# Kernel tuning notes

Hardware: AMD Instinct MI355X
Metric: run time of the kernel (lower is better)

## Reference

```python
import jax, jax.numpy as jnp
import numpy as np

DN = ('NCHW', 'OIHW', 'NCHW')
LN_EPS = 1e-5
L2_EPS = 1e-12


def dwconv(x, w, pad):
    # depthwise conv: x [b,c,h,w], w [c,1,kh,kw]
    return jax.lax.conv_general_dilated(
        x, w, (1, 1), [(pad, pad), (pad, pad)],
        dimension_numbers=DN, feature_group_count=x.shape[1])


def l2norm(x):
    n = jnp.sqrt(jnp.sum(x * x, axis=-1, keepdims=True))
    return x / jnp.maximum(n, L2_EPS)


def setup_inputs() -> dict:
    key = jax.random.key(0)
    L, c, heads, mult = 2, 512, 8, 4
    cm = c * mult
    ks = jax.random.split(key, 18)
    rn = lambda k, s, sc=0.02: jax.random.normal(k, s, jnp.float32) * sc
    return {
        'x': jax.random.normal(ks[0], (2, c, 128, 128), jnp.float32),
        'Wq': rn(ks[1], (L, c, c)),
        'Wk': rn(ks[2], (L, c, c)),
        'Wv': rn(ks[3], (L, c, c)),
        'rescale': jnp.ones((L, heads, 1, 1), jnp.float32),
        'proj_W': rn(ks[4], (L, c, c)),
        'proj_b': jnp.zeros((L, c), jnp.float32),
        'pos_w1': rn(ks[5], (L, c, 1, 3, 3)),
        'pos_w2': rn(ks[6], (L, c, 1, 3, 3)),
        'ln_g': jnp.ones((L, c), jnp.float32),
        'ln_b': jnp.zeros((L, c), jnp.float32),
        'w1': rn(ks[7], (L, cm, c)),
        'dw1': rn(ks[8], (L, cm // 4, 1, 1, 1), 0.1),
        'dw3': rn(ks[9], (L, cm // 4, 1, 3, 3), 0.1),
        'dw5': rn(ks[10], (L, cm // 4, 1, 5, 5), 0.1),
        'dw7': rn(ks[11], (L, cm // 4, 1, 7, 7), 0.1),
        'w2': rn(ks[12], (L, c, cm)),
    }


def reference(x, Wq, Wk, Wv, rescale, proj_W, proj_b, pos_w1, pos_w2,
              ln_g, ln_b, w1, dw1, dw3, dw5, dw7, w2):
    b, c, H, W = x.shape
    heads = rescale.shape[1]
    d = c // heads
    n = H * W
    x = x.transpose(0, 2, 3, 1)  # [b,H,W,c]
    for l in range(Wq.shape[0]):
        # ---- S_MSA (channel-wise transposed attention) ----
        xf = x.reshape(b, n, c)
        q_inp = xf @ Wq[l]
        k_inp = xf @ Wk[l]
        v_inp = xf @ Wv[l]
        # [b,n,heads,d] -> [b,heads,d,n]
        to_hd = lambda t: t.reshape(b, n, heads, d).transpose(0, 2, 3, 1)
        q, k, v = to_hd(q_inp), to_hd(k_inp), to_hd(v_inp)
        q = l2norm(q)
        k = l2norm(k)
        attn = jnp.einsum('bhdn,bhen->bhde', k, q) * rescale[l]  # [b,h,d,d]
        attn = jax.nn.softmax(attn, axis=-1)
        o = jnp.einsum('bhde,bhen->bhdn', attn, v)
        o = o.transpose(0, 3, 1, 2).reshape(b, n, c)  # [b,n,heads*d]
        out_c = (o @ proj_W[l] + proj_b[l]).reshape(b, H, W, c)
        # positional branch on v_inp
        vimg = v_inp.reshape(b, H, W, c).transpose(0, 3, 1, 2)
        p = dwconv(vimg, pos_w1[l], 1)
        p = jax.nn.gelu(p, approximate=False)
        p = dwconv(p, pos_w2[l], 1)
        x = x + out_c + p.transpose(0, 2, 3, 1)
        # ---- PreNorm + MS_FFN ----
        mu = x.mean(-1, keepdims=True)
        var = jnp.mean((x - mu) ** 2, axis=-1, keepdims=True)
        xn = (x - mu) / jnp.sqrt(var + LN_EPS) * ln_g[l] + ln_b[l]
        y = xn.transpose(0, 3, 1, 2)  # [b,c,H,W]
        y = jnp.einsum('oc,bchw->bohw', w1[l], y)  # [b,4c,H,W]
        y1, y2, y3, y4 = jnp.split(y, 4, axis=1)
        o1 = dwconv(y1, dw1[l], 0)
        o2 = dwconv(y2, dw3[l], 1)
        o3 = dwconv(y3, dw5[l], 2)
        o4 = dwconv(y4, dw7[l], 3)
        o = jnp.concatenate([o1, o2, o3, o4], axis=1) + y
        o = jnp.einsum('oc,bchw->bohw', w2[l], o)  # [b,c,H,W]
        x = x + o.transpose(0, 2, 3, 1)
    return x.transpose(0, 3, 1, 2)
```

## Files before the change

### kernel.cpp

```cpp
#include <hip/hip_runtime.h>
#include <math.h>

typedef unsigned short u16;
typedef short bf16x8 __attribute__((ext_vector_type(8)));
typedef float f32x4 __attribute__((ext_vector_type(4)));
typedef float f32x2 __attribute__((ext_vector_type(2)));

__device__ __forceinline__ float bf2f(u16 h) {
    union { unsigned u; float f; } v; v.u = ((unsigned)h) << 16; return v.f;
}
__device__ __forceinline__ u16 f2bf(float f) {
    union { float f; unsigned u; } v; v.f = f;
    unsigned r = v.u + 0x7fffu + ((v.u >> 16) & 1u);
    return (u16)(r >> 16);
}
__device__ __forceinline__ f32x2 up2(unsigned u) {
    union { unsigned v; float f; } lo, hi;
    lo.v = u << 16; hi.v = u & 0xffff0000u;
    f32x2 r; r.x = lo.f; r.y = hi.f; return r;
}
__device__ __forceinline__ f32x2 unpk(unsigned u) { return up2(u); }
__device__ __forceinline__ f32x4 unpk(uint2 u) {
    f32x2 a = up2(u.x), b = up2(u.y);
    f32x4 r; r.x = a.x; r.y = a.y; r.z = b.x; r.w = b.y; return r;
}
__device__ __forceinline__ unsigned pkbf(f32x2 v) {
    return (unsigned)f2bf(v.x) | ((unsigned)f2bf(v.y) << 16);
}
__device__ __forceinline__ uint2 pkbf(f32x4 v) {
    uint2 r;
    r.x = (unsigned)f2bf(v.x) | ((unsigned)f2bf(v.y) << 16);
    r.y = (unsigned)f2bf(v.z) | ((unsigned)f2bf(v.w) << 16);
    return r;
}
__device__ __forceinline__ float gl(float v) {
    return 0.5f * v * (1.f + erff(v * 0.70710678118654752f));
}

__device__ __forceinline__ void gload_lds16(const u16* g, u16* l) {
    __builtin_amdgcn_global_load_lds(
        (const __attribute__((address_space(1))) void*)g,
        (__attribute__((address_space(3))) void*)l, 16, 0, 0);
}

template<int N> struct VecT;
template<> struct VecT<2> { typedef f32x2 T; typedef unsigned U; };
template<> struct VecT<4> { typedef f32x4 T; typedef uint2 U; };

#define CH    512
#define NPIX  16384
#define PTOT  32768
#define NHEAD 8

__global__ void transpose_k(const float* __restrict__ in, float* outF, u16* outB,
                            int R, int Cc, size_t ibs, size_t obs)
{
    __shared__ float tile[32][33];
    int z = blockIdx.z;
    const float* ip = in + (size_t)z * ibs;
    int c0 = blockIdx.x * 32, r0 = blockIdx.y * 32;
    int tx = threadIdx.x, ty = threadIdx.y;
#pragma unroll
    for (int j = 0; j < 4; j++)
        tile[ty + j * 8][tx] = ip[(size_t)(r0 + ty + j * 8) * Cc + c0 + tx];
    __syncthreads();
#pragma unroll
    for (int j = 0; j < 4; j++) {
        int orow = c0 + ty + j * 8, ocol = r0 + tx;
        float v = tile[tx][ty + j * 8];
        size_t o = (size_t)z * obs + (size_t)orow * R + ocol;
        if (outF) outF[o] = v;
        if (outB) outB[o] = f2bf(v);
    }
}

__global__ void transpose16_k(const u16* __restrict__ in, u16* __restrict__ out,
                              int R, int Cc, size_t ibs, size_t obs)
{
    __shared__ u16 tile[32][34];
    int z = blockIdx.z;
    const u16* ip = in + (size_t)z * ibs;
    int c0 = blockIdx.x * 32, r0 = blockIdx.y * 32;
    int tx = threadIdx.x, ty = threadIdx.y;
#pragma unroll
    for (int j = 0; j < 4; j++)
        tile[ty + j * 8][tx] = ip[(size_t)(r0 + ty + j * 8) * Cc + c0 + tx];
    __syncthreads();
#pragma unroll
    for (int j = 0; j < 4; j++)
        out[(size_t)z * obs + (size_t)(c0 + ty + j * 8) * R + r0 + tx] = tile[tx][ty + j * 8];
}

__global__ void cvt_bf16_k(const float* __restrict__ in, u16* __restrict__ out)
{
    size_t i = ((size_t)blockIdx.x * 256 + threadIdx.x) * 4;
    float4 v = *(const float4*)&in[i];
    uint2 st;
    st.x = (unsigned)f2bf(v.x) | ((unsigned)f2bf(v.y) << 16);
    st.y = (unsigned)f2bf(v.z) | ((unsigned)f2bf(v.w) << 16);
    *(uint2*)&out[i] = st;
}

__global__ void cvtw2_k(const float* __restrict__ in, const float* __restrict__ dw1,
                        u16* __restrict__ out)
{
    size_t i = ((size_t)blockIdx.x * 256 + threadIdx.x) * 4;
    int cp = (int)(i & 2047);
    int l = (int)(i >> 20);
    int src; bool ps = false;
    if (cp < 512)       src = 1024 + cp;
    else if (cp < 1024) src = 1536 + (cp - 512);
    else if (cp < 1536) { src = cp - 1024; ps = true; }
    else                src = 512 + (cp - 1536);
    float4 v = *(const float4*)&in[(i & ~(size_t)2047) + src];
    if (ps) {
        v.x *= 1.f + dw1[l * 512 + src];
        v.y *= 1.f + dw1[l * 512 + src + 1];
        v.z *= 1.f + dw1[l * 512 + src + 2];
        v.w *= 1.f + dw1[l * 512 + src + 3];
    }
    uint2 st;
    st.x = (unsigned)f2bf(v.x) | ((unsigned)f2bf(v.y) << 16);
    st.y = (unsigned)f2bf(v.z) | ((unsigned)f2bf(v.w) << 16);
    *(uint2*)&out[i] = st;
}

__global__ __launch_bounds__(512) void gemm5_k(
    const u16* __restrict__ A, const u16* __restrict__ Bw,
    int K, int ldb, int Nn, int rowsPerBatch, int bStride, int kChunk,
    const float* __restrict__ bias, const float* resid,
    float* outF, u16* outB, const u16* __restrict__ addB)
{
    __shared__ __attribute__((aligned(16))) u16 smem[6 * 4096];
    u16* Asb = smem;
    u16* Bsb = smem + 3 * 4096;
    int tid = threadIdx.x;

    int gx = gridDim.x;
    int nwg = gx * gridDim.y;
    int lin = blockIdx.y * gx + blockIdx.x;
    int swz = lin;
    if ((nwg & 7) == 0) swz = (lin & 7) * (nwg >> 3) + (lin >> 3);
    int bx = swz % gx, by = swz / gx;

    int rowBase = by * 128, colBase = bx * 128;
    const u16* Bp = Bw + (size_t)(rowBase / rowsPerBatch) * bStride;

    int kb = 0, ke = K;
    float* outFp = outF;
    if (kChunk) {
        kb = blockIdx.z * kChunk; ke = kb + kChunk;
        outFp = outF + (size_t)blockIdx.z * (size_t)gridDim.y * 128 * Nn;
    }

    f32x4 acc[4][2] = {};
    int lane = tid & 63, wave = tid >> 6;
    int wr = wave >> 2, wc = wave & 3;
    int lm = lane & 15, lk = lane >> 4;

    int row0 = tid >> 2;
    int kc   = ((tid ^ (tid >> 3)) & 3) * 8;
    int lb0  = (tid & ~63) * 8;

    const size_t aR0 = (size_t)(rowBase + row0) * K;
    const size_t bR0 = (size_t)(colBase + row0) * ldb;

    auto STAGE = [&](int bsel, int k0) {
        gload_lds16(&A [aR0 + k0 + kc], Asb + bsel * 4096 + lb0);
        gload_lds16(&Bp[bR0 + k0 + kc], Bsb + bsel * 4096 + lb0);
    };

    const int nsteps = (ke - kb) >> 5;
    STAGE(0, kb);
    STAGE(1, kb + 32);
    const int sl = (lk ^ ((lm >> 1) & 3)) * 8;

    for (int s = 0; s < nsteps; ++s) {
        asm volatile("s_waitcnt vmcnt(2)" ::: "memory");
        __builtin_amdgcn_s_barrier();
        __builtin_amdgcn_sched_barrier(0);
        int kpf = kb + ((s + 2 < nsteps) ? (s + 2) : (nsteps - 1)) * 32;
        STAGE((s + 2) % 3, kpf);

        const u16* Ab = Asb + (s % 3) * 4096;
        const u16* Bb = Bsb + (s % 3) * 4096;
        bf16x8 af[4], bfr[2];
#pragma unroll
        for (int mt = 0; mt < 4; mt++)
            af[mt] = *(const bf16x8*)&Ab[(wr * 64 + mt * 16 + lm) * 32 + sl];
#pragma unroll
        for (int nt = 0; nt < 2; nt++)
            bfr[nt] = *(const bf16x8*)&Bb[(wc * 32 + nt * 16 + lm) * 32 + sl];
        __builtin_amdgcn_s_setprio(1);
#pragma unroll
        for (int mt = 0; mt < 4; mt++)
#pragma unroll
            for (int nt = 0; nt < 2; nt++)
                acc[mt][nt] = __builtin_amdgcn_mfma_f32_16x16x32_bf16(
                    af[mt], bfr[nt], acc[mt][nt], 0, 0, 0);
        __builtin_amdgcn_s_setprio(0);
    }

    {
        float* smf = (float*)smem;
        constexpr int PADW = 132;
        const int erow = tid >> 5;
        const int ecol = (tid & 31) * 4;
        for (int hf = 0; hf < 4; ++hf) {
            __syncthreads();
            if (wr == (hf >> 1)) {
                int mtb = (hf & 1) * 2;
#pragma unroll
                for (int m2 = 0; m2 < 2; m2++) {
#pragma unroll
                    for (int nt = 0; nt < 2; nt++) {
                        int lr = m2 * 16 + lk * 4;
                        int lc = wc * 32 + nt * 16 + lm;
#pragma unroll
                        for (int r = 0; r < 4; r++)
                            smf[(lr + r) * PADW + lc] = acc[mtb + m2][nt][r];
                    }
                }
            }
            __syncthreads();
#pragma unroll
            for (int p = 0; p < 2; p++) {
                int lrow = erow + p * 16;
                int grow = rowBase + hf * 32 + lrow;
                int gcol = colBase + ecol;
                f32x4 v = *(f32x4*)&smf[lrow * PADW + ecol];
                if (bias) {
                    v.x += bias[gcol];     v.y += bias[gcol + 1];
                    v.z += bias[gcol + 2]; v.w += bias[gcol + 3];
                }
                size_t o = (size_t)grow * Nn + gcol;
                if (resid) { f32x4 rv = *(const f32x4*)&resid[o]; v += rv; }
                if (addB)  { f32x4 av = unpk(*(const uint2*)&addB[o]); v += av; }
                if (outFp) *(f32x4*)&outFp[o] = v;
                if (outB) { uint2 pk = pkbf(v); *(uint2*)&outB[o] = pk; }
            }
        }
    }
}

template<int TM, int TN>
__global__ __launch_bounds__(256) void gemm_nt_k(
    const u16* __restrict__ A, const u16* __restrict__ Bw,
    int K, int ldb, int Nn, int rowsPerBatch, int bStride, int kChunk,
    const float* __restrict__ bias, const float* resid,
    float* outF, u16* outB, const u16* __restrict__ addB)
{
    constexpr int MT = TM / 32;
    constexpr int NT = TN / 32;
    constexpr int ABUF = TM * 32;
    constexpr int BBUF = TN * 32;
    __shared__ __attribute__((aligned(16))) u16 smem[2 * ABUF + 2 * BBUF];
    u16* Asb = smem;
    u16* Bsb = smem + 2 * ABUF;
    int tid = threadIdx.x;

    int gx = gridDim.x;
    int nwg = gx * gridDim.y;
    int lin = blockIdx.y * gx + blockIdx.x;
    int swz = lin;
    if ((nwg & 7) == 0) swz = (lin & 7) * (nwg >> 3) + (lin >> 3);
    int bx = swz % gx, by = swz / gx;

    int rowBase = by * TM, colBase = bx * TN;
    const u16* Bp = Bw + (size_t)(rowBase / rowsPerBatch) * bStride;

    int kb = 0, ke = K;
    float* outFp = outF;
    if (kChunk) {
        kb = blockIdx.z * kChunk; ke = kb + kChunk;
        outFp = outF + (size_t)blockIdx.z * (size_t)gridDim.y * TM * Nn;
    }

    f32x4 acc[MT][NT] = {};
    int lane = tid & 63, wave = tid >> 6;
    int wr = wave >> 1, wc = wave & 1;
    int lm = lane & 15, lk = lane >> 4;

    int row0 = tid >> 2;
    int kc   = ((tid ^ (tid >> 3)) & 3) * 8;
    int lb0  = (tid & ~63) * 8;

    const size_t aR0 = (size_t)(rowBase + row0) * K;
    const size_t bR0 = (size_t)(colBase + row0) * ldb;
    const size_t aR1 = (size_t)(rowBase + 64 + row0) * K;
    const size_t bR1 = (size_t)(colBase + 64 + row0) * ldb;

    auto STAGE = [&](int bsel, int k0) {
        gload_lds16(&A [aR0 + k0 + kc], Asb + bsel * ABUF + lb0);
        gload_lds16(&Bp[bR0 + k0 + kc], Bsb + bsel * BBUF + lb0);
        if constexpr (TM == 128)
            gload_lds16(&A [aR1 + k0 + kc], Asb + bsel * ABUF + lb0 + 2048);
        if constexpr (TN == 128)
            gload_lds16(&Bp[bR1 + k0 + kc], Bsb + bsel * BBUF + lb0 + 2048);
    };

    STAGE(0, kb);
    __syncthreads();
    int buf = 0;
    const int sl = (lk ^ ((lm >> 1) & 3)) * 8;

    for (int k0 = kb; k0 < ke; k0 += 32) {
        if (k0 + 32 < ke) STAGE(buf ^ 1, k0 + 32);
        const u16* Ab = Asb + buf * ABUF;
        const u16* Bb = Bsb + buf * BBUF;
        bf16x8 af[MT], bfr[NT];
#pragma unroll
        for (int mt = 0; mt < MT; mt++)
            af[mt] = *(const bf16x8*)&Ab[(wr * (TM / 2) + mt * 16 + lm) * 32 + sl];
#pragma unroll
        for (int nt = 0; nt < NT; nt++)
            bfr[nt] = *(const bf16x8*)&Bb[(wc * (TN / 2) + nt * 16 + lm) * 32 + sl];
#pragma unroll
        for (int mt = 0; mt < MT; mt++)
#pragma unroll
            for (int nt = 0; nt < NT; nt++)
                acc[mt][nt] = __builtin_amdgcn_mfma_f32_16x16x32_bf16(
                    af[mt], bfr[nt], acc[mt][nt], 0, 0, 0);
        __syncthreads();
        buf ^= 1;
    }

    {
        float* smf = (float*)smem;
        constexpr int PADW = TN + 4;
        constexpr int HALVES = TM / 32;
        constexpr int HPW = (MT / 2 > 0) ? MT / 2 : 1;
        const int erow = tid >> 5;
        const int ecol = (tid & 31) * 4;
        for (int hf = 0; hf < HALVES; ++hf) {
            __syncthreads();
            if (wr == hf / HPW) {
                int mtb = (hf % HPW) * 2;
#pragma unroll
                for (int m2 = 0; m2 < 2; m2++) {
#pragma unroll
                    for (int nt = 0; nt < NT; nt++) {
                        int lr = m2 * 16 + lk * 4;
                        int lc = wc * (TN / 2) + nt * 16 + lm;
#pragma unroll
                        for (int r = 0; r < 4; r++)
                            smf[(lr + r) * PADW + lc] = acc[mtb + m2][nt][r];
                    }
                }
            }
            __syncthreads();
#pragma unroll
            for (int p = 0; p < 4; p++) {
                int lrow = erow + p * 8;
                int grow = rowBase + hf * 32 + lrow;
                int gcol = colBase + ecol;
                f32x4 v = *(f32x4*)&smf[lrow * PADW + ecol];
                if (bias) {
                    v.x += bias[gcol];     v.y += bias[gcol + 1];
                    v.z += bias[gcol + 2]; v.w += bias[gcol + 3];
                }
                size_t o = (size_t)grow * Nn + gcol;
                if (resid) { f32x4 rv = *(const f32x4*)&resid[o]; v += rv; }
                if (addB)  { f32x4 av = unpk(*(const uint2*)&addB[o]); v += av; }
                if (outFp) *(f32x4*)&outFp[o] = v;
                if (outB) { uint2 pk = pkbf(v); *(uint2*)&outB[o] = pk; }
            }
        }
    }
}

__global__ void sreduce_k(const float* __restrict__ Sp, u16* __restrict__ Sbf)
{
    int i = blockIdx.x * 256 + threadIdx.x;
    float s = 0.f;
#pragma unroll
    for (int z = 0; z < 8; z++) s += Sp[(size_t)z * 524288 + i];
    Sbf[i] = f2bf(s);
}

__global__ void nrm_k(const float* __restrict__ w, const float* __restrict__ Tf,
                      float* __restrict__ inv)
{
    int idx = blockIdx.x * 256 + threadIdx.x;
    int e = idx & 511, b = idx >> 9;
    float s = 0.f;
    for (int c = 0; c < 512; c++)
        s += w[c * 512 + e] * Tf[(size_t)(b * 512 + c) * 512 + e];
    s = fmaxf(s, 0.f);
    inv[b * 512 + e] = 1.f / fmaxf(sqrtf(s), 1e-12f);
}

__global__ __launch_bounds__(256) void gsmall_k(
    const float* __restrict__ T2f, const float* __restrict__ Wq,
    const float* __restrict__ qinv, const float* __restrict__ kinv,
    const float* __restrict__ resc, float* __restrict__ att)
{
    __shared__ float t2l[64][64], wql[64][64];
    int t = threadIdx.x, h = blockIdx.x, b = blockIdx.y;
    const int eg = (t & 15) * 4;
    const int dg = (t >> 4) * 4;
    f32x4 acc[4] = {};
    for (int c0 = 0; c0 < 512; c0 += 64) {
        __syncthreads();
        for (int i = t; i < 4096; i += 256) {
            int cc = i >> 6, j = i & 63;
            t2l[cc][j] = T2f[(size_t)(b * 512 + c0 + cc) * 512 + h * 64 + j];
            wql[cc][j] = Wq[(size_t)(c0 + cc) * 512 + h * 64 + j];
        }
        __syncthreads();
        for (int cc = 0; cc < 64; cc++) {
            f32x4 qv = *(f32x4*)&wql[cc][eg];
            f32x4 dv = *(f32x4*)&t2l[cc][dg];
            acc[0] += dv.x * qv;
            acc[1] += dv.y * qv;
            acc[2] += dv.z * qv;
            acc[3] += dv.w * qv;
        }
    }
    float rs = resc[h];
    f32x4 qn = *(const f32x4*)&qinv[b * 512 + h * 64 + eg];
    float* ap = att + (size_t)(b * 8 + h) * 4096;
#pragma unroll
    for (int dj = 0; dj < 4; dj++) {
        int d = dg + dj;
        float kn = kinv[b * 512 + h * 64 + d];
        f32x4 v = acc[dj] * kn;
        v = v * qn;
        v.x *= rs; v.y *= rs; v.z *= rs; v.w *= rs;
        float m = fmaxf(fmaxf(v.x, v.y), fmaxf(v.z, v.w));
        for (int off = 1; off <= 8; off <<= 1) m = fmaxf(m, __shfl_xor(m, off));
        f32x4 ev;
        ev.x = expf(v.x - m); ev.y = expf(v.y - m);
        ev.z = expf(v.z - m); ev.w = expf(v.w - m);
        float s = ev.x + ev.y + ev.z + ev.w;
        for (int off = 1; off <= 8; off <<= 1) s += __shfl_xor(s, off);
        f32x4 r;
        r.x = ev.x / s; r.y = ev.y / s; r.z = ev.z / s; r.w = ev.w / s;
        *(f32x4*)&ap[d * 64 + eg] = r;
    }
}

__global__ __launch_bounds__(256) void mbuild_k(const float* __restrict__ attn,
                                                const float* __restrict__ projW,
                                                u16* Mnt)
{
    __shared__ float at[64][64];
    __shared__ float pw[64][64];
    int t = threadIdx.x;
    int h = blockIdx.x, b = blockIdx.y, ot = blockIdx.z;
    const float* ap = attn + (size_t)(b * NHEAD + h) * 4096;
    for (int i = t; i < 4096; i += 256) {
        at[i >> 6][i & 63] = ap[i];
        pw[i >> 6][i & 63] = projW[(size_t)(h * 64 + (i >> 6)) * CH + ot * 64 + (i & 63)];
    }
    __syncthreads();
    const int eg = (t & 15) * 4;
    const int rg = (t >> 4) * 4;
    f32x4 acc[4] = {};
    for (int dd = 0; dd < 64; dd++) {
        f32x4 av = *(f32x4*)&at[dd][eg];
        f32x4 pv = *(f32x4*)&pw[dd][rg];
        acc[0] += pv.x * av;
        acc[1] += pv.y * av;
        acc[2] += pv.z * av;
        acc[3] += pv.w * av;
    }
#pragma unroll
    for (int j = 0; j < 4; j++) {
        uint2 pk = pkbf(acc[j]);
        *(uint2*)&Mnt[(size_t)b * (CH * CH)
                      + (size_t)(ot * 64 + rg + j) * CH + h * 64 + eg] = pk;
    }
}

template<int KS, int YS, int CPT, bool GELU_F, bool RESID, bool ACC, int SI, int SO>
__global__ __launch_bounds__(256, 1) void dwreg_k(
    const u16* __restrict__ in, const float* __restrict__ w,
    u16* __restrict__ outB, float* __restrict__ outAdd)
{
    constexpr int PAD = KS / 2;
    typedef typename VecT<CPT>::T fv;
    typedef typename VecT<CPT>::U uv;
    const int tid = threadIdx.x;
    const int cbase = (CPT == 4) ? ((tid & 127) * 4) : (tid * 2);
    const int x     = (CPT == 4) ? ((int)blockIdx.x * 2 + (tid >> 7)) : (int)blockIdx.x;
    const int y0 = blockIdx.y * YS;
    const int b  = blockIdx.z;
    const size_t bi = (size_t)b * NPIX * SI + cbase;
    const size_t bo = (size_t)b * NPIX * SO + cbase;

    fv wv[KS * KS];
#pragma unroll
    for (int t = 0; t < KS * KS; t++) {
        fv vv;
        vv.x = w[(cbase + 0) * KS * KS + t];
        vv.y = w[(cbase + 1) * KS * KS + t];
        if constexpr (CPT == 4) {
            vv.z = w[(cbase + 2) * KS * KS + t];
            vv.w = w[(cbase + 3) * KS * KS + t];
        }
        wv[t] = vv;
    }

    fv win[KS][KS];
    uv tmp[KS];

    auto rowload = [&](int t) {
        int yy = y0 - PAD + t;
        bool rv = ((unsigned)yy < 128u);
#pragma unroll
        for (int kx = 0; kx < KS; kx++) {
            int xx = x + kx - PAD;
            uv u = {};
            if (rv && ((unsigned)xx < 128u))
                u = *(const uv*)&in[bi + ((size_t)yy * 128 + xx) * SI];
            tmp[kx] = u;
        }
    };
    auto unpackrow = [&](int slot) {
#pragma unroll
        for (int kx = 0; kx < KS; kx++) win[slot][kx] = unpk(tmp[kx]);
    };

#pragma unroll
    for (int t = 0; t < KS - 1; t++) { rowload(t); unpackrow(t); }
    rowload(KS - 1);

    for (int i0 = 0; i0 < YS; i0 += KS) {
#pragma unroll
        for (int j = 0; j < KS; j++) {
            int i = i0 + j;
            if (i >= YS) break;
            unpackrow((j + KS - 1) % KS);
            if (i < YS - 1) rowload(i + KS);
            fv r = {};
#pragma unroll
            for (int ky = 0; ky < KS; ky++)
#pragma unroll
                for (int kx = 0; kx < KS; kx++)
                    r += win[(j + ky) % KS][kx] * wv[ky * KS + kx];
            if (GELU_F) {
                r.x = gl(r.x); r.y = gl(r.y);
                if constexpr (CPT == 4) { r.z = gl(r.z); r.w = gl(r.w); }
            }
            if (RESID) r += win[(j + PAD) % KS][PAD];
            size_t opos = bo + ((size_t)(y0 + i) * 128 + x) * SO;
            if (ACC) {
                fv* p = (fv*)&outAdd[opos];
                *p = *p + r;
            } else {
                uv pk = pkbf(r);
                *(uv*)&outB[opos] = pk;
            }
        }
    }
}

__global__ void ln_k(const float* __restrict__ xf, const float* __restrict__ g,
                     const float* __restrict__ bb, u16* __restrict__ xn)
{
    int t = threadIdx.x, lane = t & 63, wv = t >> 6;
    size_t pix = (size_t)blockIdx.x * 4 + wv;
    const float* row = xf + pix * CH;
    float4 a = *(const float4*)&row[lane * 8];
    float4 c = *(const float4*)&row[lane * 8 + 4];
    float s = a.x + a.y + a.z + a.w + c.x + c.y + c.z + c.w;
    float sq = a.x * a.x + a.y * a.y + a.z * a.z + a.w * a.w
             + c.x * c.x + c.y * c.y + c.z * c.z + c.w * c.w;
    for (int off = 32; off; off >>= 1) {
        s  += __shfl_xor(s, off);
        sq += __shfl_xor(sq, off);
    }
    float mu = s * (1.f / 512.f);
    float var = fmaxf(sq * (1.f / 512.f) - mu * mu, 0.f);
    float inv = rsqrtf(var + 1e-5f);
    float vals[8] = {a.x, a.y, a.z, a.w, c.x, c.y, c.z, c.w};
    unsigned o[4];
#pragma unroll
    for (int j = 0; j < 4; j++) {
        int cix = lane * 8 + j * 2;
        float v0 = (vals[j * 2] - mu) * inv * g[cix] + bb[cix];
        float v1 = (vals[j * 2 + 1] - mu) * inv * g[cix + 1] + bb[cix + 1];
        o[j] = (unsigned)f2bf(v0) | ((unsigned)f2bf(v1) << 16);
    }
    *(uint4*)&xn[pix * CH + lane * 8] = make_uint4(o[0], o[1], o[2], o[3]);
}

extern "C" void kernel_launch(void* const* d_in, const int* in_sizes, int n_in,
                              void* d_out, int out_size, void* d_ws, size_t ws_size,
                              hipStream_t stream)
{
    (void)in_sizes; (void)n_in; (void)out_size; (void)ws_size;
    const float* x_in  = (const float*)d_in[0];
    const float* Wq    = (const float*)d_in[1];
    const float* Wk    = (const float*)d_in[2];
    const float* Wv    = (const float*)d_in[3];
    const float* resc  = (const float*)d_in[4];
    const float* projW = (const float*)d_in[5];
    const float* projB = (const float*)d_in[6];
    const float* posw1 = (const float*)d_in[7];
    const float* posw2 = (const float*)d_in[8];
    const float* lng   = (const float*)d_in[9];
    const float* lnb   = (const float*)d_in[10];
    const float* w1    = (const float*)d_in[11];
    const float* dw1   = (const float*)d_in[12];
    const float* dw3   = (const float*)d_in[13];
    const float* dw5   = (const float*)d_in[14];
    const float* dw7   = (const float*)d_in[15];
    const float* w2    = (const float*)d_in[16];
    float* out = (float*)d_out;
    char* ws = (char*)d_ws;

    float* XF  = (float*)(ws + 0);
    u16*   XBb = (u16*)  (ws + 67108864ull);
    u16*   WQt = (u16*)  (ws + 100663296ull);
    u16*   WKt = (u16*)  (ws + 101711872ull);
    u16*   WVt = (u16*)  (ws + 102760448ull);
    u16*   W1b = (u16*)  (ws + 103809024ull);
    u16*   W2b = (u16*)  (ws + 108003328ull);
    u16*   Mnt = (u16*)  (ws + 112197632ull);
    u16*   Sbf = (u16*)  (ws + 113246208ull);
    float* T1f = (float*)(ws + 114294784ull);
    float* T2f = (float*)(ws + 116391936ull);
    float* QNI = (float*)(ws + 118489088ull);
    float* KNI = (float*)(ws + 118493184ull);
    float* ATT = (float*)(ws + 118497280ull);

    u16*   R2  = (u16*)d_out;
    u16*   R3  = (u16*)d_out + 16777216;
    float* Sp  = (float*)((char*)d_out + 33554432ull);
    u16*   Y2  = (u16*)d_out;

    const int BIG = 1 << 30;
    dim3 tb(32, 8);

    transpose_k<<<dim3(512, 16, 2), tb, 0, stream>>>(x_in, XF, XBb, 512, 16384, 8388608, 8388608);
    transpose_k<<<dim3(16, 16, 2), tb, 0, stream>>>(Wq, nullptr, WQt, 512, 512, 262144, 262144);
    transpose_k<<<dim3(16, 16, 2), tb, 0, stream>>>(Wk, nullptr, WKt, 512, 512, 262144, 262144);
    transpose_k<<<dim3(16, 16, 2), tb, 0, stream>>>(Wv, nullptr, WVt, 512, 512, 262144, 262144);
    cvt_bf16_k<<<2048, 256, 0, stream>>>(w1, W1b);
    cvtw2_k<<<2048, 256, 0, stream>>>(w2, dw1, W2b);

    for (int l = 0; l < 2; l++) {
        if (l == 0)
            cvt_bf16_k<<<16384, 256, 0, stream>>>(x_in, R2);
        else
            transpose16_k<<<dim3(16, 512, 2), tb, 0, stream>>>(XBb, R2, 16384, 512, 8388608, 8388608);
        gemm5_k<<<dim3(4, 8, 8), 512, 0, stream>>>(R2, R2, 16384, 16384, 512,
            512, 8388608, 2048, nullptr, nullptr, Sp, nullptr, nullptr);
        sreduce_k<<<2048, 256, 0, stream>>>(Sp, Sbf);
        gemm_nt_k<64, 128><<<dim3(4, 16), 256, 0, stream>>>(Sbf, WQt + l * 262144, 512, 512, 512,
            BIG, 0, 0, nullptr, nullptr, T1f, nullptr, nullptr);
        gemm_nt_k<64, 128><<<dim3(4, 16), 256, 0, stream>>>(Sbf, WKt + l * 262144, 512, 512, 512,
            BIG, 0, 0, nullptr, nullptr, T2f, nullptr, nullptr);
        nrm_k<<<8, 256, 0, stream>>>(Wq + l * 262144, T1f, QNI);
        nrm_k<<<8, 256, 0, stream>>>(Wk + l * 262144, T2f, KNI);
        gsmall_k<<<dim3(8, 2), 256, 0, stream>>>(T2f, Wq + l * 262144, QNI, KNI,
            resc + l * 8, ATT);
        mbuild_k<<<dim3(8, 2, 8), 256, 0, stream>>>(ATT, projW + l * 262144, Mnt);
        gemm5_k<<<dim3(4, 256), 512, 0, stream>>>(XBb, WVt + l * 262144, 512, 512, 512,
            BIG, 0, 0, nullptr, nullptr, nullptr, R3, nullptr);
        dwreg_k<3, 16, 4, true, false, false, 512, 512><<<dim3(64, 8, 2), 256, 0, stream>>>(
            R3, posw1 + l * 4608, R2, nullptr);
        dwreg_k<3, 16, 4, false, false, false, 512, 512><<<dim3(64, 8, 2), 256, 0, stream>>>(
            R2, posw2 + l * 4608, XBb, nullptr);
        gemm5_k<<<dim3(4, 256), 512, 0, stream>>>(R3, Mnt, 512, 512, 512,
            16384, 262144, 0, projB + l * 512, XF, XF, nullptr, XBb);
        ln_k<<<8192, 256, 0, stream>>>(XF, lng + l * 512, lnb + l * 512, XBb);
        for (int b2 = 0; b2 < 2; b2++) {
            const size_t boff = (size_t)b2 * NPIX * 512;
            const u16* w1l = W1b + l * 1048576;
            gemm5_k<<<dim3(8, 128), 512, 0, stream>>>(XBb + boff,
                w1l + 2 * 262144, 512, 512, 2048,
                BIG, 0, 0, nullptr, nullptr, nullptr, Y2 + 1024, nullptr);
            dwreg_k<5, 16, 2, false, true, false, 2048, 2048><<<dim3(128, 8, 1), 256, 0, stream>>>(
                Y2 + 1024, dw5 + l * 12800, Y2 + 0, nullptr);
            dwreg_k<7, 32, 2, false, true, false, 2048, 2048><<<dim3(128, 4, 1), 256, 0, stream>>>(
                Y2 + 1536, dw7 + l * 25088, Y2 + 512, nullptr);
            gemm5_k<<<dim3(4, 128), 512, 0, stream>>>(XBb + boff,
                w1l + 1 * 262144, 512, 512, 2048,
                BIG, 0, 0, nullptr, nullptr, nullptr, Y2 + 1024, nullptr);
            dwreg_k<3, 16, 4, false, true, false, 2048, 2048><<<dim3(64, 8, 1), 256, 0, stream>>>(
                Y2 + 1024, dw3 + l * 4608, Y2 + 1536, nullptr);
            gemm5_k<<<dim3(4, 128), 512, 0, stream>>>(XBb + boff,
                w1l + 0 * 262144, 512, 512, 2048,
                BIG, 0, 0, nullptr, nullptr, nullptr, Y2 + 1024, nullptr);
            gemm5_k<<<dim3(4, 128), 512, 0, stream>>>(Y2,
                W2b + l * 1048576, 2048, 2048, 512,
                BIG, 0, 0, nullptr, XF + boff, XF + boff, XBb + boff, nullptr);
        }
    }
    transpose_k<<<dim3(16, 512, 2), tb, 0, stream>>>(XF, out, nullptr, 16384, 512, 8388608, 8388608);
}
```

Before: 1.496 ms.

## Merge Q/K small GEMMs, double split-K for Gram, prefetch epilogue operands

Concatenates transposed Wq and Wk into one buffer so a single small GEMM produces T1 and T2 side by side, and fuses the two norm kernels into one launch. Doubles the split-K factor of the Gram GEMM (16 chunks of 1024) to expose more blocks, with sreduce summing 16 partials. In the gemm5 epilogue, bias is hoisted out of the loop and resid/addB loads are issued before the barrier, with lighter s_barrier synchronisation. This cuts launch count and hides epilogue load latency, but adds extra partial-sum traffic and relies on T12f aliasing the Sp region of the output buffer.

```diff
diff --git a/kernel.cpp b/kernel.cpp
--- a/kernel.cpp
+++ b/kernel.cpp
@@ -206,8 +206,19 @@
         constexpr int PADW = 132;
         const int erow = tid >> 5;
         const int ecol = (tid & 31) * 4;
+        const int gcol = colBase + ecol;
+        f32x4 bv = {};
+        if (bias) {
+            bv.x = bias[gcol];     bv.y = bias[gcol + 1];
+            bv.z = bias[gcol + 2]; bv.w = bias[gcol + 3];
+        }
         for (int hf = 0; hf < 4; ++hf) {
-            __syncthreads();
+            if (hf == 0) {
+                __syncthreads();
+            } else {
+                asm volatile("s_waitcnt lgkmcnt(0)" ::: "memory");
+                __builtin_amdgcn_s_barrier();
+            }
             if (wr == (hf >> 1)) {
                 int mtb = (hf & 1) * 2;
 #pragma unroll
@@ -222,22 +233,23 @@
                     }
                 }
             }
-            __syncthreads();
-#pragma unroll
-            for (int p = 0; p < 2; p++) {
-                int lrow = erow + p * 16;
-                int grow = rowBase + hf * 32 + lrow;
-                int gcol = colBase + ecol;
-                f32x4 v = *(f32x4*)&smf[lrow * PADW + ecol];
-                if (bias) {
-                    v.x += bias[gcol];     v.y += bias[gcol + 1];
-                    v.z += bias[gcol + 2]; v.w += bias[gcol + 3];
-                }
-                size_t o = (size_t)grow * Nn + gcol;
-                if (resid) { f32x4 rv = *(const f32x4*)&resid[o]; v += rv; }
-                if (addB)  { f32x4 av = unpk(*(const uint2*)&addB[o]); v += av; }
-                if (outFp) *(f32x4*)&outFp[o] = v;
-                if (outB) { uint2 pk = pkbf(v); *(uint2*)&outB[o] = pk; }
+            int r0 = rowBase + hf * 32 + erow, r1 = r0 + 16;
+            size_t o0 = (size_t)r0 * Nn + gcol, o1 = (size_t)r1 * Nn + gcol;
+            f32x4 rv0 = {}, rv1 = {};
+            uint2 av0 = {}, av1 = {};
+            if (resid) { rv0 = *(const f32x4*)&resid[o0]; rv1 = *(const f32x4*)&resid[o1]; }
+            if (addB)  { av0 = *(const uint2*)&addB[o0];  av1 = *(const uint2*)&addB[o1]; }
+            asm volatile("s_waitcnt lgkmcnt(0)" ::: "memory");
+            __builtin_amdgcn_s_barrier();
+            f32x4 v0 = *(f32x4*)&smf[erow * PADW + ecol];
+            f32x4 v1 = *(f32x4*)&smf[(erow + 16) * PADW + ecol];
+            v0 += bv; v1 += bv;
+            if (resid) { v0 += rv0; v1 += rv1; }
+            if (addB)  { v0 += unpk(av0); v1 += unpk(av1); }
+            if (outFp) { *(f32x4*)&outFp[o0] = v0; *(f32x4*)&outFp[o1] = v1; }
+            if (outB) {
+                uint2 p0 = pkbf(v0), p1 = pkbf(v1);
+                *(uint2*)&outB[o0] = p0; *(uint2*)&outB[o1] = p1;
             }
         }
     }
@@ -374,20 +386,24 @@
     int i = blockIdx.x * 256 + threadIdx.x;
     float s = 0.f;
 #pragma unroll
-    for (int z = 0; z < 8; z++) s += Sp[(size_t)z * 524288 + i];
+    for (int z = 0; z < 16; z++) s += Sp[(size_t)z * 524288 + i];
     Sbf[i] = f2bf(s);
 }
 
-__global__ void nrm_k(const float* __restrict__ w, const float* __restrict__ Tf,
-                      float* __restrict__ inv)
+__global__ void nrm_k(const float* __restrict__ Wqf, const float* __restrict__ Wkf,
+                      const float* __restrict__ T12f,
+                      float* __restrict__ QNI, float* __restrict__ KNI)
 {
     int idx = blockIdx.x * 256 + threadIdx.x;
-    int e = idx & 511, b = idx >> 9;
+    int e = idx & 511, b = (idx >> 9) & 1, which = idx >> 10;
+    const float* w = which ? Wkf : Wqf;
+    const float* Tf = T12f + which * 512;
     float s = 0.f;
     for (int c = 0; c < 512; c++)
-        s += w[c * 512 + e] * Tf[(size_t)(b * 512 + c) * 512 + e];
+        s += w[c * 512 + e] * Tf[(size_t)(b * 512 + c) * 1024 + e];
     s = fmaxf(s, 0.f);
-    inv[b * 512 + e] = 1.f / fmaxf(sqrtf(s), 1e-12f);
+    float* outp = which ? KNI : QNI;
+    outp[b * 512 + e] = 1.f / fmaxf(sqrtf(s), 1e-12f);
 }
 
 __global__ __launch_bounds__(256) void gsmall_k(
@@ -404,7 +420,7 @@
         __syncthreads();
         for (int i = t; i < 4096; i += 256) {
             int cc = i >> 6, j = i & 63;
-            t2l[cc][j] = T2f[(size_t)(b * 512 + c0 + cc) * 512 + h * 64 + j];
+            t2l[cc][j] = T2f[(size_t)(b * 512 + c0 + cc) * 1024 + h * 64 + j];
             wql[cc][j] = Wq[(size_t)(c0 + cc) * 512 + h * 64 + j];
         }
         __syncthreads();
@@ -613,15 +629,12 @@
 
     float* XF  = (float*)(ws + 0);
     u16*   XBb = (u16*)  (ws + 67108864ull);
-    u16*   WQt = (u16*)  (ws + 100663296ull);
-    u16*   WKt = (u16*)  (ws + 101711872ull);
+    u16*   WQK = (u16*)  (ws + 100663296ull);
     u16*   WVt = (u16*)  (ws + 102760448ull);
     u16*   W1b = (u16*)  (ws + 103809024ull);
     u16*   W2b = (u16*)  (ws + 108003328ull);
     u16*   Mnt = (u16*)  (ws + 112197632ull);
     u16*   Sbf = (u16*)  (ws + 113246208ull);
-    float* T1f = (float*)(ws + 114294784ull);
-    float* T2f = (float*)(ws + 116391936ull);
     float* QNI = (float*)(ws + 118489088ull);
     float* KNI = (float*)(ws + 118493184ull);
     float* ATT = (float*)(ws + 118497280ull);
@@ -629,14 +642,15 @@
     u16*   R2  = (u16*)d_out;
     u16*   R3  = (u16*)d_out + 16777216;
     float* Sp  = (float*)((char*)d_out + 33554432ull);
+    float* T12f= (float*)((char*)d_out + 33554432ull);
     u16*   Y2  = (u16*)d_out;
 
     const int BIG = 1 << 30;
     dim3 tb(32, 8);
 
     transpose_k<<<dim3(512, 16, 2), tb, 0, stream>>>(x_in, XF, XBb, 512, 16384, 8388608, 8388608);
-    transpose_k<<<dim3(16, 16, 2), tb, 0, stream>>>(Wq, nullptr, WQt, 512, 512, 262144, 262144);
-    transpose_k<<<dim3(16, 16, 2), tb, 0, stream>>>(Wk, nullptr, WKt, 512, 512, 262144, 262144);
+    transpose_k<<<dim3(16, 16, 2), tb, 0, stream>>>(Wq, nullptr, WQK, 512, 512, 262144, 524288);
+    transpose_k<<<dim3(16, 16, 2), tb, 0, stream>>>(Wk, nullptr, WQK + 262144, 512, 512, 262144, 524288);
     transpose_k<<<dim3(16, 16, 2), tb, 0, stream>>>(Wv, nullptr, WVt, 512, 512, 262144, 262144);
     cvt_bf16_k<<<2048, 256, 0, stream>>>(w1, W1b);
     cvtw2_k<<<2048, 256, 0, stream>>>(w2, dw1, W2b);
@@ -646,16 +660,13 @@
             cvt_bf16_k<<<16384, 256, 0, stream>>>(x_in, R2);
         else
             transpose16_k<<<dim3(16, 512, 2), tb, 0, stream>>>(XBb, R2, 16384, 512, 8388608, 8388608);
-        gemm5_k<<<dim3(4, 8, 8), 512, 0, stream>>>(R2, R2, 16384, 16384, 512,
-            512, 8388608, 2048, nullptr, nullptr, Sp, nullptr, nullptr);
+        gemm5_k<<<dim3(4, 8, 16), 512, 0, stream>>>(R2, R2, 16384, 16384, 512,
+            512, 8388608, 1024, nullptr, nullptr, Sp, nullptr, nullptr);
         sreduce_k<<<2048, 256, 0, stream>>>(Sp, Sbf);
-        gemm_nt_k<64, 128><<<dim3(4, 16), 256, 0, stream>>>(Sbf, WQt + l * 262144, 512, 512, 512,
-            BIG, 0, 0, nullptr, nullptr, T1f, nullptr, nullptr);
-        gemm_nt_k<64, 128><<<dim3(4, 16), 256, 0, stream>>>(Sbf, WKt + l * 262144, 512, 512, 512,
-            BIG, 0, 0, nullptr, nullptr, T2f, nullptr, nullptr);
-        nrm_k<<<8, 256, 0, stream>>>(Wq + l * 262144, T1f, QNI);
-        nrm_k<<<8, 256, 0, stream>>>(Wk + l * 262144, T2f, KNI);
-        gsmall_k<<<dim3(8, 2), 256, 0, stream>>>(T2f, Wq + l * 262144, QNI, KNI,
+        gemm_nt_k<64, 128><<<dim3(8, 16), 256, 0, stream>>>(Sbf, WQK + l * 524288,
+            512, 512, 1024, BIG, 0, 0, nullptr, nullptr, T12f, nullptr, nullptr);
+        nrm_k<<<8, 256, 0, stream>>>(Wq + l * 262144, Wk + l * 262144, T12f, QNI, KNI);
+        gsmall_k<<<dim3(8, 2), 256, 0, stream>>>(T12f + 512, Wq + l * 262144, QNI, KNI,
             resc + l * 8, ATT);
         mbuild_k<<<dim3(8, 2, 8), 256, 0, stream>>>(ATT, projW + l * 262144, Mnt);
         gemm5_k<<<dim3(4, 256), 512, 0, stream>>>(XBb, WVt + l * 262144, 512, 512, 512,
```

New measurement: 1.404 ms. -6.2%, faster.
